# Kernel tuning notes

Hardware: AMD Instinct MI355X
Metric: run time of the kernel (lower is better)

Reference implementation:

```python
import jax, jax.numpy as jnp
import numpy as np
import math

H = 1024  # hidden_dim
NH = 16   # num_heads
HD = H // NH  # head_dim = 64
B, S, C = 2, 2048, 256  # batch, seq_len, cond_len
EPS = 1e-5


def layernorm(x, g, b):
    m = jnp.mean(x, axis=-1, keepdims=True)
    v = jnp.var(x, axis=-1, keepdims=True)
    return (x - m) * jax.lax.rsqrt(v + EPS) * g + b


def apply_rope(x, freqs):
    # x: [b, s, h, d], freqs broadcastable to [b, s, h, d//2]
    cos, sin = jnp.cos(freqs), jnp.sin(freqs)
    x1, x2 = jnp.split(x, 2, axis=-1)
    return jnp.concatenate([x1 * cos - x2 * sin, x2 * cos + x1 * sin], axis=-1)


def setup_inputs() -> dict:
    key = jax.random.key(0)
    ks = jax.random.split(key, 16)
    sc = 0.02
    x = jax.random.normal(ks[0], (B, S, H), jnp.float32)
    # rope freqs: positions * inv_freq over half head dim
    inv_freq = 1.0 / (10000.0 ** (jnp.arange(HD // 2, dtype=jnp.float32) / (HD // 2)))
    rope_freqs = (jnp.arange(S, dtype=jnp.float32)[:, None] * inv_freq[None, :]).reshape(S, 1, HD // 2)
    # causal additive mask [1,1,S,S]
    causal = jnp.tril(jnp.ones((S, S), dtype=bool))
    attention_mask = jnp.where(causal, 0.0, -1e9).astype(jnp.float32)[None, None]
    conditioning = jax.random.normal(ks[1], (B, C, H), jnp.float32)
    conditioning_mask = jnp.zeros((B, 1, 1, C), jnp.float32)
    params = dict(
        ln1_g=jnp.ones((H,)), ln1_b=jnp.zeros((H,)),
        ln2_g=jnp.ones((H,)), ln2_b=jnp.zeros((H,)),
        lnc_g=jnp.ones((H,)), lnc_b=jnp.zeros((H,)),
        w_qkv=jax.random.normal(ks[2], (H, 3 * H)) * sc,
        w_out=jax.random.normal(ks[3], (H, H)) * sc, b_out=jnp.zeros((H,)),
        w_cq=jax.random.normal(ks[4], (H, H)) * sc,
        w_ckv=jax.random.normal(ks[5], (H, 2 * H)) * sc,
        w_cout=jax.random.normal(ks[6], (H, H)) * sc, b_cout=jnp.zeros((H,)),
        w_ff1=jax.random.normal(ks[7], (H, 4 * H)) * sc, b_ff1=jnp.zeros((4 * H,)),
        w_ff2=jax.random.normal(ks[8], (4 * H, H)) * sc, b_ff2=jnp.zeros((H,)),
    )
    return dict(x=x, rope_freqs=rope_freqs, attention_mask=attention_mask,
                conditioning=conditioning, conditioning_mask=conditioning_mask, **params)


def reference(x, rope_freqs, attention_mask, conditioning, conditioning_mask,
              ln1_g, ln1_b, ln2_g, ln2_b, lnc_g, lnc_b,
              w_qkv, w_out, b_out, w_cq, w_ckv, w_cout, b_cout,
              w_ff1, b_ff1, w_ff2, b_ff2):
    scale = 1.0 / math.sqrt(HD)
    # --- causal self-attention ---
    residual = x
    h = layernorm(x, ln1_g, ln1_b)
    qkv = h @ w_qkv  # [b,s,3H]
    q, k, v = jnp.split(qkv, 3, axis=-1)
    q = q.reshape(B, S, NH, HD)
    k = k.reshape(B, S, NH, HD)
    v = v.reshape(B, S, NH, HD)
    q = apply_rope(q, rope_freqs)
    k = apply_rope(k, rope_freqs)
    scores = jnp.einsum('bqhd,bkhd->bhqk', q, k) * scale + attention_mask
    attn = jax.nn.softmax(scores, axis=-1)
    out = jnp.einsum('bhqk,bkhd->bqhd', attn, v).reshape(B, S, H)
    x = residual + out @ w_out + b_out
    # --- cross-attention ---
    residual = x
    h = layernorm(x, lnc_g, lnc_b)
    q = (h @ w_cq).reshape(B, S, NH, HD)
    kv = conditioning @ w_ckv
    k, v = jnp.split(kv, 2, axis=-1)
    k = k.reshape(B, C, NH, HD)
    v = v.reshape(B, C, NH, HD)
    scores = jnp.einsum('bqhd,bkhd->bhqk', q, k) * scale + conditioning_mask
    attn = jax.nn.softmax(scores, axis=-1)
    out = jnp.einsum('bhqk,bkhd->bqhd', attn, v).reshape(B, S, H)
    x = residual + out @ w_cout + b_cout
    # --- FFN ---
    residual = x
    h = layernorm(x, ln2_g, ln2_b)
    h = jax.nn.gelu(h @ w_ff1 + b_ff1, approximate=False)
    x = residual + h @ w_ff2 + b_ff2
    return x
```

## Files before the change

### kernel.cpp

```cpp
#include <hip/hip_runtime.h>

#define HDIM   1024
#define NHEADS 16
#define HEADD  64
#define BATCH  2
#define SEQ    2048
#define CLEN   256
#define NROWS  (BATCH*SEQ)
#define SCALE  0.125f
#define LOG2E  1.44269504088896f

typedef __bf16 bf16x8 __attribute__((ext_vector_type(8)));
typedef float  f32x4  __attribute__((ext_vector_type(4)));

__device__ __forceinline__ unsigned short f2bf(float f) {
  union { __bf16 b; unsigned short u; } x;
  x.b = (__bf16)f;
  return x.u;
}
__device__ __forceinline__ float bf2f(unsigned short u) {
  union { unsigned int u; float f; } x; x.u = ((unsigned int)u) << 16;
  return x.f;
}

__device__ __forceinline__ void gl2lds16(const unsigned short* g, unsigned short* l) {
  __builtin_amdgcn_global_load_lds(
      (const __attribute__((address_space(1))) unsigned int*)g,
      (__attribute__((address_space(3))) unsigned int*)l, 16, 0, 0);
}

template<int VM> __device__ __forceinline__ void wait_vm_barrier() {
  if constexpr (VM == 0)      asm volatile("s_waitcnt vmcnt(0)\n\ts_barrier" ::: "memory");
  else if constexpr (VM == 2) asm volatile("s_waitcnt vmcnt(2)\n\ts_barrier" ::: "memory");
  else if constexpr (VM == 3) asm volatile("s_waitcnt vmcnt(3)\n\ts_barrier" ::: "memory");
  else if constexpr (VM == 4) asm volatile("s_waitcnt vmcnt(4)\n\ts_barrier" ::: "memory");
  else                        asm volatile("s_waitcnt vmcnt(6)\n\ts_barrier" ::: "memory");
}
__device__ __forceinline__ void bar_only() { asm volatile("s_barrier" ::: "memory"); }

struct CastTab { const float* s[8]; unsigned short* d[8]; };

__global__ __launch_bounds__(256)
void cast_fused(CastTab tab) {
  __shared__ float t[64][68];
  const int bid = blockIdx.x;
  const int tid = threadIdx.x;
  int w, base, K, N;
  if      (bid < 768)  { w = 0; base = 0;    K = 1024; N = 3072; }
  else if (bid < 1024) { w = 1; base = 768;  K = 1024; N = 1024; }
  else if (bid < 1280) { w = 2; base = 1024; K = 1024; N = 1024; }
  else if (bid < 1792) { w = 3; base = 1280; K = 1024; N = 2048; }
  else if (bid < 2048) { w = 4; base = 1792; K = 1024; N = 1024; }
  else if (bid < 3072) { w = 5; base = 2048; K = 1024; N = 4096; }
  else if (bid < 4096) { w = 6; base = 3072; K = 4096; N = 1024; }
  else                 { w = 7; base = 4096; K = 0;    N = 0;    }
  if (w == 7) {
    const float* in = tab.s[7];
    unsigned short* out = tab.d[7];
    int i = (bid - base) * 256 + tid;
    float4 a = ((const float4*)in)[2 * i], bq = ((const float4*)in)[2 * i + 1];
    unsigned short us[8] = { f2bf(a.x),  f2bf(a.y),  f2bf(a.z),  f2bf(a.w),
                             f2bf(bq.x), f2bf(bq.y), f2bf(bq.z), f2bf(bq.w) };
    ((uint4*)out)[i] = *(uint4*)us;
    return;
  }
  const float* in = tab.s[w];
  unsigned short* out = tab.d[w];
  const int lb = bid - base;
  const int tilesX = N >> 6;
  const int bx = lb % tilesX, by = lb / tilesX;
  const int kb = by * 64, nb = bx * 64;
  const int r = tid >> 4, c = (tid & 15) * 4;
#pragma unroll
  for (int i = 0; i < 4; ++i) {
    float4 v = *(const float4*)(in + (size_t)(kb + r + i * 16) * N + nb + c);
    t[r + i * 16][c]     = v.x;
    t[r + i * 16][c + 1] = v.y;
    t[r + i * 16][c + 2] = v.z;
    t[r + i * 16][c + 3] = v.w;
  }
  __syncthreads();
  const int nr = tid >> 3, kc = (tid & 7) * 8;
#pragma unroll
  for (int i = 0; i < 2; ++i) {
    unsigned short us[8];
#pragma unroll
    for (int j = 0; j < 8; ++j) us[j] = f2bf(t[kc + j][nr + i * 32]);
    *(uint4*)(out + (size_t)(nb + nr + i * 32) * K + kb + kc) = *(uint4*)us;
  }
}

__global__ __launch_bounds__(256)
void vtrans_kernel(const unsigned short* __restrict__ in, int str, int voff, int rows,
                   unsigned short* __restrict__ out) {
  __shared__ unsigned short t[64][72];
  const int h = blockIdx.y & (NHEADS - 1), b = blockIdx.y >> 4;
  const int s0 = blockIdx.x * 64;
  const int tid = threadIdx.x;
  const int r = tid >> 2, c = (tid & 3) * 16;
  const unsigned short* src = in + (size_t)(b * rows + s0 + r) * str + voff + h * 64 + c;
  *(uint4*)(&t[r][c])     = *(const uint4*)(src);
  *(uint4*)(&t[r][c + 8]) = *(const uint4*)(src + 8);
  __syncthreads();
  const int d = tid >> 2, sc = (tid & 3) * 16;
  unsigned short tmp[16];
#pragma unroll
  for (int i = 0; i < 16; ++i) tmp[i] = t[sc + i][d];
  unsigned short* dst = out + ((size_t)(b * NHEADS + h) * 64 + d) * rows + s0 + sc;
  *(uint4*)(dst)     = *(uint4*)(tmp);
  *(uint4*)(dst + 8) = *(uint4*)(tmp + 8);
}

__global__ __launch_bounds__(256)
void layernorm_kernel(const float* __restrict__ x, const float* __restrict__ g,
                      const float* __restrict__ b, unsigned short* __restrict__ out) {
  int row = blockIdx.x;
  const float4 v = ((const float4*)(x + (size_t)row * HDIM))[threadIdx.x];
  float s  = v.x + v.y + v.z + v.w;
  float sq = v.x*v.x + v.y*v.y + v.z*v.z + v.w*v.w;
  for (int o = 32; o; o >>= 1) { s += __shfl_xor(s, o); sq += __shfl_xor(sq, o); }
  __shared__ float rs[4], rq[4];
  int wave = threadIdx.x >> 6;
  if ((threadIdx.x & 63) == 0) { rs[wave] = s; rq[wave] = sq; }
  __syncthreads();
  s  = rs[0] + rs[1] + rs[2] + rs[3];
  sq = rq[0] + rq[1] + rq[2] + rq[3];
  float mean = s * (1.f/HDIM);
  float var  = sq * (1.f/HDIM) - mean*mean;
  float rstd = rsqrtf(var + 1e-5f);
  float4 gg = ((const float4*)g)[threadIdx.x];
  float4 bb = ((const float4*)b)[threadIdx.x];
  ushort4 o;
  o.x = f2bf((v.x - mean) * rstd * gg.x + bb.x);
  o.y = f2bf((v.y - mean) * rstd * gg.y + bb.y);
  o.z = f2bf((v.z - mean) * rstd * gg.z + bb.z);
  o.w = f2bf((v.w - mean) * rstd * gg.w + bb.w);
  ((ushort4*)(out + (size_t)row * HDIM))[threadIdx.x] = o;
}

__global__ __launch_bounds__(256)
void layernorm_bf16_kernel(const unsigned short* __restrict__ x, const float* __restrict__ g,
                           const float* __restrict__ b, unsigned short* __restrict__ out) {
  int row = blockIdx.x;
  ushort4 uv = ((const ushort4*)(x + (size_t)row * HDIM))[threadIdx.x];
  float v0 = bf2f(uv.x), v1 = bf2f(uv.y), v2 = bf2f(uv.z), v3 = bf2f(uv.w);
  float s  = v0 + v1 + v2 + v3;
  float sq = v0*v0 + v1*v1 + v2*v2 + v3*v3;
  for (int o = 32; o; o >>= 1) { s += __shfl_xor(s, o); sq += __shfl_xor(sq, o); }
  __shared__ float rs[4], rq[4];
  int wave = threadIdx.x >> 6;
  if ((threadIdx.x & 63) == 0) { rs[wave] = s; rq[wave] = sq; }
  __syncthreads();
  s  = rs[0] + rs[1] + rs[2] + rs[3];
  sq = rq[0] + rq[1] + rq[2] + rq[3];
  float mean = s * (1.f/HDIM);
  float var  = sq * (1.f/HDIM) - mean*mean;
  float rstd = rsqrtf(var + 1e-5f);
  float4 gg = ((const float4*)g)[threadIdx.x];
  float4 bb = ((const float4*)b)[threadIdx.x];
  ushort4 o;
  o.x = f2bf((v0 - mean) * rstd * gg.x + bb.x);
  o.y = f2bf((v1 - mean) * rstd * gg.y + bb.y);
  o.z = f2bf((v2 - mean) * rstd * gg.z + bb.z);
  o.w = f2bf((v3 - mean) * rstd * gg.w + bb.w);
  ((ushort4*)(out + (size_t)row * HDIM))[threadIdx.x] = o;
}

template<int TBM, int TBN, int DEPTH, bool BIAS, bool RES, bool RESBF, bool GELU_, bool OUTBF>
__global__ __launch_bounds__(512)
void gemm_bt(const unsigned short* __restrict__ A, const unsigned short* __restrict__ Bt,
             const float* __restrict__ bias, const void* __restrict__ res,
             void* __restrict__ out, int M, int N, int K) {
  constexpr int MR = TBM / 32;
  constexpr int NR = TBN / 64;
  constexpr int AIS = TBM / 64;
  constexpr int BIS = TBN / 64;
  constexpr int LOADS = AIS + BIS;
  constexpr int NBUF = DEPTH + 1;
  __shared__ unsigned short Al[NBUF][TBM * 64];
  __shared__ unsigned short Bl[NBUF][TBN * 64];
  const int tid  = threadIdx.x;
  const int wave = tid >> 6, lane = tid & 63;
  const int wr = wave >> 2, wc = wave & 3;
  const int nwg = gridDim.x * gridDim.y;
  int lin = blockIdx.y * gridDim.x + blockIdx.x;
  lin = (lin & 7) * (nwg >> 3) + (lin >> 3);
  const int m0 = (lin / gridDim.x) * TBM, n0 = (lin % gridDim.x) * TBN;
  const int lrow = lane & 15, hi = lane >> 4;
  const int rx = lrow & 7;

  f32x4 acc[MR][NR] = {};

  const int trow = tid >> 3, pslot = tid & 7;
  const int lcol = (pslot ^ (trow & 7)) * 8;
  const unsigned short* ga = A  + (size_t)(m0 + trow) * K + lcol;
  const unsigned short* gb = Bt + (size_t)(n0 + trow) * K + lcol;
  const int ldst = trow * 64 + pslot * 8;
  const int nt = K >> 6;

  auto stage = [&](int buf, int t) {
    const int k = t << 6;
#pragma unroll
    for (int i = 0; i < AIS; ++i)
      gl2lds16(ga + (size_t)i * 64 * K + k, Al[buf] + ldst + i * 64 * 64);
#pragma unroll
    for (int i = 0; i < BIS; ++i)
      gl2lds16(gb + (size_t)i * 64 * K + k, Bl[buf] + ldst + i * 64 * 64);
  };
  auto compute = [&](int c) {
#pragma unroll
    for (int kk = 0; kk < 2; ++kk) {
      const int cslot = ((kk << 2) | hi);
      const int coff  = (cslot ^ rx) * 8;
      bf16x8 af[MR], bfr[NR];
#pragma unroll
      for (int m = 0; m < MR; ++m)
        af[m] = *(const bf16x8*)(Al[c] + (wr*(TBM/2) + m*16 + lrow) * 64 + coff);
#pragma unroll
      for (int n = 0; n < NR; ++n)
        bfr[n] = *(const bf16x8*)(Bl[c] + (wc*(TBN/4) + n*16 + lrow) * 64 + coff);
#pragma unroll
      for (int m = 0; m < MR; ++m)
#pragma unroll
        for (int n = 0; n < NR; ++n)
          acc[m][n] = __builtin_amdgcn_mfma_f32_16x16x32_bf16(af[m], bfr[n], acc[m][n], 0, 0, 0);
    }
  };

  stage(0, 0);
  if constexpr (DEPTH == 2) stage(1, 1);
  int cur = 0;
  for (int t = 0; t < nt - DEPTH; ++t) {
    int nb = cur + DEPTH; if (nb >= NBUF) nb -= NBUF;
    stage(nb, t + DEPTH);
    wait_vm_barrier<DEPTH * LOADS>();
    compute(cur);
    bar_only();
    cur = (cur + 1 == NBUF) ? 0 : cur + 1;
  }
  if constexpr (DEPTH == 2) {
    wait_vm_barrier<LOADS>();
    compute(cur);
    bar_only();
    cur = (cur + 1 == NBUF) ? 0 : cur + 1;
  }
  wait_vm_barrier<0>();
  compute(cur);

#pragma unroll
  for (int m = 0; m < MR; ++m)
#pragma unroll
    for (int n = 0; n < NR; ++n)
#pragma unroll
      for (int r = 0; r < 4; ++r) {
        int row = m0 + wr*(TBM/2) + m*16 + hi * 4 + r;
        int col = n0 + wc*(TBN/4) + n*16 + lrow;
        float v = acc[m][n][r];
        if (BIAS)  v += bias[col];
        if (GELU_) v = 0.5f * v * (1.0f + erff(v * 0.70710678118654752f));
        if (RES) {
          if constexpr (RESBF) v += bf2f(((const unsigned short*)res)[(size_t)row * N + col]);
          else                 v += ((const float*)res)[(size_t)row * N + col];
        }
        if (OUTBF) ((unsigned short*)out)[(size_t)row * N + col] = f2bf(v);
        else       ((float*)out)[(size_t)row * N + col] = v;
      }
}

__global__ void rope_kernel(unsigned short* __restrict__ qkv, const float* __restrict__ freqs) {
  int idx = blockIdx.x * 256 + threadIdx.x;
  int d = idx & 31;
  int h = (idx >> 5) & 15;
  int row = idx >> 9;
  int s = row & (SEQ - 1);
  float f = freqs[s * 32 + d];
  float sn, cs;
  sincosf(f, &sn, &cs);
  size_t base = (size_t)row * 3072 + h * 64 + d;
  float x1 = bf2f(qkv[base]), x2 = bf2f(qkv[base + 32]);
  qkv[base]      = f2bf(x1 * cs - x2 * sn);
  qkv[base + 32] = f2bf(x2 * cs + x1 * sn);
  float y1 = bf2f(qkv[base + 1024]), y2 = bf2f(qkv[base + 1024 + 32]);
  qkv[base + 1024]      = f2bf(y1 * cs - y2 * sn);
  qkv[base + 1024 + 32] = f2bf(y2 * cs + y1 * sn);
}

__global__ __launch_bounds__(512)
void flash_attn_causal8(const unsigned short* __restrict__ qp, int qstr,
                        const unsigned short* __restrict__ kp, int kstr,
                        const unsigned short* __restrict__ vt,
                        unsigned short* __restrict__ outp) {
  __shared__ unsigned short Kl[2][64 * 64];
  __shared__ unsigned short Vl[2][64 * 64];
  __shared__ unsigned short Pl[8][16][72];

  const int id = blockIdx.y * gridDim.x + blockIdx.x;
  const int bh = (id & 7) * 4 + ((id >> 3) & 3);
  const int qpair = id >> 5;
  const int h = bh & (NHEADS - 1), b = bh >> 4;

  const int tid = threadIdx.x;
  const int wave = tid >> 6, lane = tid & 63;
  const int grp = wave >> 2, w4 = wave & 3;
  const int lo = lane & 15, hi = lane >> 4;
  const int NQB = SEQ / 64;
  const float SC2 = SCALE * LOG2E;
  float* mb = (float*)&Pl[0][0][0];

  bf16x8 onesf;
#pragma unroll
  for (int j = 0; j < 8; ++j) onesf[j] = (__bf16)1.0f;

  const unsigned short* vbase = vt + (size_t)(b * NHEADS + h) * 64 * SEQ;
  const int g256 = tid & 255;
  const int trow = g256 >> 3, pslot = g256 & 7;
  const int lcol = (pslot ^ (trow & 7)) * 8;
  const int ldst = g256 * 8;
  const int x7 = lo & 7;
  const int c0 = (hi ^ x7) * 8, c1 = ((hi + 4) ^ x7) * 8;

  for (int pass = 0; pass < 2; ++pass) {
    const int qblk = pass == 0 ? qpair : NQB - 1 - qpair;
    const int q0 = qblk * 64;
    const int qw = q0 + w4 * 16;

    bf16x8 qf[2];
    {
      const unsigned short* qb = qp + (size_t)(b * SEQ + qw + lo) * qstr + h * 64 + hi * 8;
      qf[0] = *(const bf16x8*)(qb);
      qf[1] = *(const bf16x8*)(qb + 32);
#pragma unroll
      for (int j = 0; j < 8; ++j) {
        qf[0][j] = (__bf16)((float)qf[0][j] * SC2);
        qf[1][j] = (__bf16)((float)qf[1][j] * SC2);
      }
    }

    f32x4 o_acc[4] = {};
    f32x4 l_acc = {};
    float mrow[4];
#pragma unroll
    for (int r = 0; r < 4; ++r) mrow[r] = -1e30f;

    const int T = qblk + 1;
    const int iters = (T + 1) >> 1;
    for (int it = 0; it < iters; ++it) {
      const int t = 2 * it + grp;
      const bool act = t < T;
      const int j0 = t * 64;
      if (act) {
        const unsigned short* ks = kp + (size_t)(b * SEQ + j0 + trow) * kstr + h * 64 + lcol;
        const unsigned short* vs = vbase + (size_t)trow * SEQ + j0 + lcol;
        gl2lds16(ks, Kl[grp] + ldst);
        gl2lds16(ks + (size_t)32 * kstr, Kl[grp] + ldst + 32 * 64);
        gl2lds16(vs, Vl[grp] + ldst);
        gl2lds16(vs + (size_t)32 * SEQ, Vl[grp] + ldst + 32 * 64);
      }
      __syncthreads();
      if (act) {
        const unsigned short* Kc = Kl[grp];
        const unsigned short* Vc = Vl[grp];
        f32x4 s[4] = {};
#pragma unroll
        for (int n = 0; n < 4; ++n) {
          bf16x8 b0 = *(const bf16x8*)(Kc + (n * 16 + lo) * 64 + c0);
          bf16x8 b1 = *(const bf16x8*)(Kc + (n * 16 + lo) * 64 + c1);
          s[n] = __builtin_amdgcn_mfma_f32_16x16x32_bf16(qf[0], b0, s[n], 0, 0, 0);
          s[n] = __builtin_amdgcn_mfma_f32_16x16x32_bf16(qf[1], b1, s[n], 0, 0, 0);
        }
        if (t == T - 1) {
#pragma unroll
          for (int n = 0; n < 4; ++n)
#pragma unroll
            for (int r = 0; r < 4; ++r)
              if (j0 + n * 16 + lo > qw + hi * 4 + r) s[n][r] = -1e30f;
        }
        float pr[4][4];
#pragma unroll
        for (int r = 0; r < 4; ++r) {
          float mx = fmaxf(fmaxf(s[0][r], s[1][r]), fmaxf(s[2][r], s[3][r]));
          mx = fmaxf(mx, __shfl_xor(mx, 1));
          mx = fmaxf(mx, __shfl_xor(mx, 2));
          mx = fmaxf(mx, __shfl_xor(mx, 4));
          mx = fmaxf(mx, __shfl_xor(mx, 8));
          const float mnew = fmaxf(mrow[r], mx);
          const float corr = exp2f(mrow[r] - mnew);
          mrow[r] = mnew;
          l_acc[r] *= corr;
#pragma unroll
          for (int n = 0; n < 4; ++n)
            pr[n][r] = exp2f(s[n][r] - mnew);
#pragma unroll
          for (int n2 = 0; n2 < 4; ++n2) o_acc[n2][r] *= corr;
        }
#pragma unroll
        for (int n = 0; n < 4; ++n)
#pragma unroll
          for (int r = 0; r < 4; ++r)
            Pl[wave][hi * 4 + r][n * 16 + lo] = f2bf(pr[n][r]);

        bf16x8 pa0 = *(const bf16x8*)(&Pl[wave][lo][hi * 8]);
        bf16x8 pa1 = *(const bf16x8*)(&Pl[wave][lo][32 + hi * 8]);
        l_acc = __builtin_amdgcn_mfma_f32_16x16x32_bf16(pa0, onesf, l_acc, 0, 0, 0);
        l_acc = __builtin_amdgcn_mfma_f32_16x16x32_bf16(pa1, onesf, l_acc, 0, 0, 0);
#pragma unroll
        for (int n = 0; n < 4; ++n) {
          bf16x8 vb0 = *(const bf16x8*)(Vc + (n * 16 + lo) * 64 + c0);
          bf16x8 vb1 = *(const bf16x8*)(Vc + (n * 16 + lo) * 64 + c1);
          o_acc[n] = __builtin_amdgcn_mfma_f32_16x16x32_bf16(pa0, vb0, o_acc[n], 0, 0, 0);
          o_acc[n] = __builtin_amdgcn_mfma_f32_16x16x32_bf16(pa1, vb1, o_acc[n], 0, 0, 0);
        }
      }
      __syncthreads();
    }

    unsigned short* ob = outp + (size_t)(b * SEQ + qw) * HDIM + h * 64;
#pragma unroll
    for (int half = 0; half < 2; ++half) {
      __syncthreads();
      if (grp == 1) {
        float* dst = mb + (w4 * 64 + lane) * 13;
#pragma unroll
        for (int rr = 0; rr < 2; ++rr) {
          int r = half * 2 + rr;
          dst[rr * 6]     = mrow[r];
          dst[rr * 6 + 1] = l_acc[r];
#pragma unroll
          for (int n = 0; n < 4; ++n) dst[rr * 6 + 2 + n] = o_acc[n][r];
        }
      }
      __syncthreads();
      if (grp == 0) {
        const float* s1 = mb + (w4 * 64 + lane) * 13;
#pragma unroll
        for (int rr = 0; rr < 2; ++rr) {
          int r = half * 2 + rr;
          float m1 = s1[rr * 6], l1 = s1[rr * 6 + 1];
          float M  = fmaxf(mrow[r], m1);
          float c0f = exp2f(mrow[r] - M), c1f = exp2f(m1 - M);
          float inv = 1.f / (l_acc[r] * c0f + l1 * c1f);
#pragma unroll
          for (int n = 0; n < 4; ++n) {
            float o = o_acc[n][r] * c0f + s1[rr * 6 + 2 + n] * c1f;
            ob[(size_t)(hi * 4 + r) * HDIM + n * 16 + lo] = f2bf(o * inv);
          }
        }
      }
    }
    __syncthreads();
  }
}

__global__ __launch_bounds__(256)
void flash_attn_cross(const unsigned short* __restrict__ qp, int qstr,
                      const unsigned short* __restrict__ kp, int kstr,
                      const unsigned short* __restrict__ vt,
                      int kvrows,
                      unsigned short* __restrict__ outp) {
  __shared__ unsigned short Kl[2][64 * 64];
  __shared__ unsigned short Vl[2][64 * 64];
  __shared__ unsigned short Pl[4][16][72];

  const int id = blockIdx.y * gridDim.x + blockIdx.x;
  const int bh = (id & 7) * 4 + ((id >> 3) & 3);
  const int qblk = id >> 5;
  const int h = bh & (NHEADS - 1), b = bh >> 4;

  const int tid = threadIdx.x;
  const int wave = tid >> 6, lane = tid & 63;
  const int lo = lane & 15, hi = lane >> 4;
  const float SC2 = SCALE * LOG2E;

  bf16x8 onesf;
#pragma unroll
  for (int j = 0; j < 8; ++j) onesf[j] = (__bf16)1.0f;

  const unsigned short* vbase = vt + (size_t)(b * NHEADS + h) * 64 * kvrows;
  const int trow = tid >> 3, pslot = tid & 7;
  const int lcol = (pslot ^ (trow & 7)) * 8;
  const int ldst = tid * 8;
  const int x7 = lo & 7;
  const int c0 = (hi ^ x7) * 8, c1 = ((hi + 4) ^ x7) * 8;

  const int qw = qblk * 64 + wave * 16;

  bf16x8 qf[2];
  {
    const unsigned short* qb = qp + (size_t)(b * SEQ + qw + lo) * qstr + h * 64 + hi * 8;
    qf[0] = *(const bf16x8*)(qb);
    qf[1] = *(const bf16x8*)(qb + 32);
#pragma unroll
    for (int j = 0; j < 8; ++j) {
      qf[0][j] = (__bf16)((float)qf[0][j] * SC2);
      qf[1][j] = (__bf16)((float)qf[1][j] * SC2);
    }
  }

  f32x4 o_acc[4] = {};
  f32x4 l_acc = {};
  float mrow[4];
#pragma unroll
  for (int r = 0; r < 4; ++r) mrow[r] = -1e30f;

  auto stageKV = [&](int buf, int t) {
    const int j = t * 64;
    const unsigned short* ks = kp + (size_t)(b * kvrows + j + trow) * kstr + h * 64 + lcol;
    const unsigned short* vs = vbase + (size_t)trow * kvrows + j + lcol;
    gl2lds16(ks, Kl[buf] + ldst);
    gl2lds16(ks + (size_t)32 * kstr, Kl[buf] + ldst + 32 * 64);
    gl2lds16(vs, Vl[buf] + ldst);
    gl2lds16(vs + (size_t)32 * kvrows, Vl[buf] + ldst + 32 * 64);
  };
  auto computeTile = [&](int c) {
    const unsigned short* Kc = Kl[c];
    const unsigned short* Vc = Vl[c];
    f32x4 s[4] = {};
#pragma unroll
    for (int n = 0; n < 4; ++n) {
      bf16x8 b0 = *(const bf16x8*)(Kc + (n * 16 + lo) * 64 + c0);
      bf16x8 b1 = *(const bf16x8*)(Kc + (n * 16 + lo) * 64 + c1);
      s[n] = __builtin_amdgcn_mfma_f32_16x16x32_bf16(qf[0], b0, s[n], 0, 0, 0);
      s[n] = __builtin_amdgcn_mfma_f32_16x16x32_bf16(qf[1], b1, s[n], 0, 0, 0);
    }
    float pr[4][4];
#pragma unroll
    for (int r = 0; r < 4; ++r) {
      float mx = fmaxf(fmaxf(s[0][r], s[1][r]), fmaxf(s[2][r], s[3][r]));
      mx = fmaxf(mx, __shfl_xor(mx, 1));
      mx = fmaxf(mx, __shfl_xor(mx, 2));
      mx = fmaxf(mx, __shfl_xor(mx, 4));
      mx = fmaxf(mx, __shfl_xor(mx, 8));
      const float mnew = fmaxf(mrow[r], mx);
      const float corr = exp2f(mrow[r] - mnew);
      mrow[r] = mnew;
      l_acc[r] *= corr;
#pragma unroll
      for (int n = 0; n < 4; ++n)
        pr[n][r] = exp2f(s[n][r] - mnew);
#pragma unroll
      for (int n2 = 0; n2 < 4; ++n2) o_acc[n2][r] *= corr;
    }
#pragma unroll
    for (int n = 0; n < 4; ++n)
#pragma unroll
      for (int r = 0; r < 4; ++r)
        Pl[wave][hi * 4 + r][n * 16 + lo] = f2bf(pr[n][r]);
    bf16x8 pa0 = *(const bf16x8*)(&Pl[wave][lo][hi * 8]);
    bf16x8 pa1 = *(const bf16x8*)(&Pl[wave][lo][32 + hi * 8]);
    l_acc = __builtin_amdgcn_mfma_f32_16x16x32_bf16(pa0, onesf, l_acc, 0, 0, 0);
    l_acc = __builtin_amdgcn_mfma_f32_16x16x32_bf16(pa1, onesf, l_acc, 0, 0, 0);
#pragma unroll
    for (int n = 0; n < 4; ++n) {
      bf16x8 vb0 = *(const bf16x8*)(Vc + (n * 16 + lo) * 64 + c0);
      bf16x8 vb1 = *(const bf16x8*)(Vc + (n * 16 + lo) * 64 + c1);
      o_acc[n] = __builtin_amdgcn_mfma_f32_16x16x32_bf16(pa0, vb0, o_acc[n], 0, 0, 0);
      o_acc[n] = __builtin_amdgcn_mfma_f32_16x16x32_bf16(pa1, vb1, o_acc[n], 0, 0, 0);
    }
  };

  const int T = kvrows / 64;
  stageKV(0, 0);
  int cur = 0;
  for (int t = 0; t < T - 1; ++t) {
    stageKV(cur ^ 1, t + 1);
    wait_vm_barrier<4>();
    computeTile(cur);
    bar_only();
    cur ^= 1;
  }
  wait_vm_barrier<0>();
  computeTile(cur);

  unsigned short* ob = outp + (size_t)(b * SEQ + qw) * HDIM + h * 64;
#pragma unroll
  for (int r = 0; r < 4; ++r) {
    const float inv = 1.f / l_acc[r];
#pragma unroll
    for (int n = 0; n < 4; ++n)
      ob[(size_t)(hi * 4 + r) * HDIM + n * 16 + lo] = f2bf(o_acc[n][r] * inv);
  }
}

extern "C" void kernel_launch(void* const* d_in, const int* in_sizes, int n_in,
                              void* d_out, int out_size, void* d_ws, size_t ws_size,
                              hipStream_t stream) {
  const float* x      = (const float*)d_in[0];
  const float* rfreq  = (const float*)d_in[1];
  const float* cond   = (const float*)d_in[3];
  const float* ln1_g  = (const float*)d_in[5];
  const float* ln1_b  = (const float*)d_in[6];
  const float* ln2_g  = (const float*)d_in[7];
  const float* ln2_b  = (const float*)d_in[8];
  const float* lnc_g  = (const float*)d_in[9];
  const float* lnc_b  = (const float*)d_in[10];
  const float* w_qkv  = (const float*)d_in[11];
  const float* w_out  = (const float*)d_in[12];
  const float* b_out  = (const float*)d_in[13];
  const float* w_cq   = (const float*)d_in[14];
  const float* w_ckv  = (const float*)d_in[15];
  const float* w_cout = (const float*)d_in[16];
  const float* b_cout = (const float*)d_in[17];
  const float* w_ff1  = (const float*)d_in[18];
  const float* b_ff1  = (const float*)d_in[19];
  const float* w_ff2  = (const float*)d_in[20];
  const float* b_ff2  = (const float*)d_in[21];

  char* ws = (char*)d_ws;
  size_t off = 0;
  auto alloc = [&](size_t bytes) { size_t r = off; off += (bytes + 255) & ~(size_t)255; return r; };
  unsigned short* wt_qkv  = (unsigned short*)(ws + alloc((size_t)3072*1024*2));
  unsigned short* wt_out  = (unsigned short*)(ws + alloc((size_t)1024*1024*2));
  unsigned short* wt_cq   = (unsigned short*)(ws + alloc((size_t)1024*1024*2));
  unsigned short* wt_ckv  = (unsigned short*)(ws + alloc((size_t)2048*1024*2));
  unsigned short* wt_cout = (unsigned short*)(ws + alloc((size_t)1024*1024*2));
  unsigned short* wt_ff1  = (unsigned short*)(ws + alloc((size_t)4096*1024*2));
  unsigned short* wt_ff2  = (unsigned short*)(ws + alloc((size_t)1024*4096*2));
  unsigned short* condb   = (unsigned short*)(ws + alloc((size_t)512*1024*2));
  unsigned short* hbuf    = (unsigned short*)(ws + alloc((size_t)NROWS*1024*2));
  unsigned short* big     = (unsigned short*)(ws + alloc((size_t)NROWS*4096*2));
  unsigned short* attnb   = (unsigned short*)(ws + alloc((size_t)NROWS*1024*2));
  unsigned short* x1b     = (unsigned short*)(ws + alloc((size_t)NROWS*1024*2));
  unsigned short* kvc     = (unsigned short*)(ws + alloc((size_t)512*2048*2));
  unsigned short* vts     = (unsigned short*)(ws + alloc((size_t)BATCH*NHEADS*64*SEQ*2));
  unsigned short* vtc     = (unsigned short*)(ws + alloc((size_t)BATCH*NHEADS*64*CLEN*2));
  float*          outf    = (float*)d_out;

  CastTab tab;
  tab.s[0] = w_qkv;  tab.d[0] = wt_qkv;
  tab.s[1] = w_out;  tab.d[1] = wt_out;
  tab.s[2] = w_cq;   tab.d[2] = wt_cq;
  tab.s[3] = w_ckv;  tab.d[3] = wt_ckv;
  tab.s[4] = w_cout; tab.d[4] = wt_cout;
  tab.s[5] = w_ff1;  tab.d[5] = wt_ff1;
  tab.s[6] = w_ff2;  tab.d[6] = wt_ff2;
  tab.s[7] = cond;   tab.d[7] = condb;
  cast_fused<<<4352, 256, 0, stream>>>(tab);

  layernorm_kernel<<<NROWS, 256, 0, stream>>>(x, ln1_g, ln1_b, hbuf);
  gemm_bt<128,128,1,false,false,false,false,true><<<dim3(3072/128, NROWS/128), 512, 0, stream>>>(
      hbuf, wt_qkv, nullptr, nullptr, big, NROWS, 3072, 1024);
  rope_kernel<<<(NROWS*NHEADS*32)/256, 256, 0, stream>>>(big, rfreq);
  vtrans_kernel<<<dim3(SEQ/64, BATCH*NHEADS), 256, 0, stream>>>(big, 3072, 2048, SEQ, vts);
  flash_attn_causal8<<<dim3(SEQ/64/2, BATCH*NHEADS), 512, 0, stream>>>(
      big, 3072, big + 1024, 3072, vts, attnb);
  gemm_bt<128,64,2,true,true,false,false,true><<<dim3(1024/64, NROWS/128), 512, 0, stream>>>(
      attnb, wt_out, b_out, x, x1b, NROWS, 1024, 1024);

  layernorm_bf16_kernel<<<NROWS, 256, 0, stream>>>(x1b, lnc_g, lnc_b, hbuf);
  gemm_bt<128,64,2,false,false,false,false,true><<<dim3(1024/64, NROWS/128), 512, 0, stream>>>(
      hbuf, wt_cq, nullptr, nullptr, big, NROWS, 1024, 1024);
  gemm_bt<64,64,2,false,false,false,false,true><<<dim3(2048/64, 512/64), 512, 0, stream>>>(
      condb, wt_ckv, nullptr, nullptr, kvc, 512, 2048, 1024);
  vtrans_kernel<<<dim3(CLEN/64, BATCH*NHEADS), 256, 0, stream>>>(kvc, 2048, 1024, CLEN, vtc);
  flash_attn_cross<<<dim3(SEQ/64, BATCH*NHEADS), 256, 0, stream>>>(
      big, 1024, kvc, 2048, vtc, CLEN, attnb);
  gemm_bt<128,64,2,true,true,true,false,false><<<dim3(1024/64, NROWS/128), 512, 0, stream>>>(
      attnb, wt_cout, b_cout, x1b, outf, NROWS, 1024, 1024);

  layernorm_kernel<<<NROWS, 256, 0, stream>>>(outf, ln2_g, ln2_b, hbuf);
  gemm_bt<128,128,1,true,false,false,true,true><<<dim3(4096/128, NROWS/128), 512, 0, stream>>>(
      hbuf, wt_ff1, b_ff1, nullptr, big, NROWS, 4096, 1024);
  gemm_bt<128,64,2,true,true,false,false,false><<<dim3(1024/64, NROWS/128), 512, 0, stream>>>(
      big, wt_ff2, b_ff2, outf, outf, NROWS, 1024, 4096);
}
```

Before: 313.6 us.

## Double-buffer K tiles and overlap V loads with QK^T in causal flash attention

Adds a second K buffer per group so the next K tile is prefetched during the current iteration, and issues the V load before the QK^T and softmax stage, waiting on it only before the PV MFMAs. Fine-grained vmcnt waits replace the full syncthreads, so global-to-LDS latency should hide behind compute in the causal self-attention kernel. This costs extra LDS per block, which may lower occupancy, and inactive groups now issue redundant clamped loads.

```diff
diff --git a/kernel.cpp b/kernel.cpp
--- a/kernel.cpp
+++ b/kernel.cpp
@@ -290,7 +290,7 @@
                         const unsigned short* __restrict__ kp, int kstr,
                         const unsigned short* __restrict__ vt,
                         unsigned short* __restrict__ outp) {
-  __shared__ unsigned short Kl[2][64 * 64];
+  __shared__ unsigned short Kl[2][2][64 * 64];
   __shared__ unsigned short Vl[2][64 * 64];
   __shared__ unsigned short Pl[8][16][72];
 
@@ -321,8 +321,7 @@
 
   for (int pass = 0; pass < 2; ++pass) {
     const int qblk = pass == 0 ? qpair : NQB - 1 - qpair;
-    const int q0 = qblk * 64;
-    const int qw = q0 + w4 * 16;
+    const int qw = qblk * 64 + w4 * 16;
 
     bf16x8 qf[2];
     {
@@ -344,22 +343,33 @@
 
     const int T = qblk + 1;
     const int iters = (T + 1) >> 1;
+    const int tmax = T - 1;
+
+    auto stageK = [&](int buf, int t) {
+      const unsigned short* ks = kp + (size_t)(b * SEQ + t * 64 + trow) * kstr + h * 64 + lcol;
+      gl2lds16(ks, Kl[grp][buf] + ldst);
+      gl2lds16(ks + (size_t)32 * kstr, Kl[grp][buf] + ldst + 32 * 64);
+    };
+    auto stageV = [&](int t) {
+      const unsigned short* vs = vbase + (size_t)trow * SEQ + t * 64 + lcol;
+      gl2lds16(vs, Vl[grp] + ldst);
+      gl2lds16(vs + (size_t)32 * SEQ, Vl[grp] + ldst + 32 * 64);
+    };
+
+    stageK(0, grp < T ? grp : tmax);
+    int buf = 0;
     for (int it = 0; it < iters; ++it) {
       const int t = 2 * it + grp;
       const bool act = t < T;
-      const int j0 = t * 64;
+      const int tc = act ? t : tmax;
+      stageV(tc);
+      int tk = t + 2; if (tk > tmax) tk = tmax;
+      stageK(buf ^ 1, tk);
+      wait_vm_barrier<4>();
+
       if (act) {
-        const unsigned short* ks = kp + (size_t)(b * SEQ + j0 + trow) * kstr + h * 64 + lcol;
-        const unsigned short* vs = vbase + (size_t)trow * SEQ + j0 + lcol;
-        gl2lds16(ks, Kl[grp] + ldst);
-        gl2lds16(ks + (size_t)32 * kstr, Kl[grp] + ldst + 32 * 64);
-        gl2lds16(vs, Vl[grp] + ldst);
-        gl2lds16(vs + (size_t)32 * SEQ, Vl[grp] + ldst + 32 * 64);
-      }
-      __syncthreads();
-      if (act) {
-        const unsigned short* Kc = Kl[grp];
-        const unsigned short* Vc = Vl[grp];
+        const int j0 = t * 64;
+        const unsigned short* Kc = Kl[grp][buf];
         f32x4 s[4] = {};
 #pragma unroll
         for (int n = 0; n < 4; ++n) {
@@ -398,7 +408,12 @@
 #pragma unroll
           for (int r = 0; r < 4; ++r)
             Pl[wave][hi * 4 + r][n * 16 + lo] = f2bf(pr[n][r]);
-
+      }
+
+      wait_vm_barrier<2>();
+
+      if (act) {
+        const unsigned short* Vc = Vl[grp];
         bf16x8 pa0 = *(const bf16x8*)(&Pl[wave][lo][hi * 8]);
         bf16x8 pa1 = *(const bf16x8*)(&Pl[wave][lo][32 + hi * 8]);
         l_acc = __builtin_amdgcn_mfma_f32_16x16x32_bf16(pa0, onesf, l_acc, 0, 0, 0);
@@ -411,7 +426,8 @@
           o_acc[n] = __builtin_amdgcn_mfma_f32_16x16x32_bf16(pa1, vb1, o_acc[n], 0, 0, 0);
         }
       }
-      __syncthreads();
+      bar_only();
+      buf ^= 1;
     }
 
     unsigned short* ob = outp + (size_t)(b * SEQ + qw) * HDIM + h * 64;
```

New measurement: 313.8 us. Within noise of the previous version (+0.1%).
